# Kernel tuning notes

Measured on AMD Instinct MI355X. Metric: run time of the kernel, lower is better.

## Reference

```python
import jax, jax.numpy as jnp
import numpy as np

N_NODES = 50000
D_IN = 128
D_OUT = 64
N_ETYPES = 3
E_PER_ETYPE = 500000
P_ETYPE = 0.5  # self.p[etype] init value for every etype


def setup_inputs() -> dict:
    key = jax.random.key(0)
    k1, k2, k3, k4 = jax.random.split(key, 4)
    feat = jax.random.normal(k1, (N_NODES, D_IN), dtype=jnp.float32)
    W = jax.random.normal(k2, (D_IN, D_OUT), dtype=jnp.float32) * 0.05
    b = jax.random.normal(k3, (D_OUT,), dtype=jnp.float32) * 0.05
    # edge_index[e] = (src, dst) for etype e
    edge_index = jax.random.randint(k4, (N_ETYPES, 2, E_PER_ETYPE), 0, N_NODES, dtype=jnp.int64)
    return {"feat": feat, "W": W, "b": b, "edge_index": edge_index}


def reference(feat, W, b, edge_index):
    N = feat.shape[0]

    def agg_one_etype(ei):
        src, dst = ei[0], ei[1]
        # scatter-mean of src features onto dst nodes (dgl copy_u + mean)
        msg_sum = jax.ops.segment_sum(feat[src], dst, num_segments=N)          # [N, D]
        cnt = jax.ops.segment_sum(jnp.ones(src.shape, feat.dtype), dst, num_segments=N)
        hr = msg_sum / jnp.maximum(cnt, 1.0)[:, None]  # zero-in-degree nodes -> 0
        return jnp.tanh(hr)  # per-etype activation

    hr_all = jax.vmap(agg_one_etype)(edge_index)        # [n_etypes, N, D]
    h_homo = jnp.sum(hr_all * P_ETYPE, axis=0) + feat   # weighted sum + residual
    h_homo = jnp.tanh(h_homo)
    return h_homo @ W + b                               # final linear
```

## Files before the change

### kernel.cpp

```cpp
#include <hip/hip_runtime.h>
#include <hip/hip_bf16.h>

#define N_NODES 50000
#define D_IN 128
#define D_OUT 64
#define N_ETYPES 3
#define E_PER_ETYPE 500000
#define N_EDGES (N_ETYPES * E_PER_ETYPE)
#define CAP1 16
#define CAP2 30
#define DMAX (CAP1 + CAP2)
#define ZROW N_NODES
#define NB_FEAT ((N_NODES * D_IN / 4) / 256)
#define NB_W ((D_IN * D_OUT) / 256)
#define NB_ZCNT 147
#define CHUNK_EDGES 2048
#define N_CHUNKS ((N_EDGES + CHUNK_EDGES - 1) / CHUNK_EDGES)

typedef __attribute__((ext_vector_type(8))) short short8;
typedef __attribute__((ext_vector_type(4))) float f32x4;

static __device__ __forceinline__ unsigned short f2bf(float f) {
    unsigned int x = __float_as_uint(f);
    unsigned int lsb = (x >> 16) & 1u;
    x += 0x7fffu + lsb;
    return (unsigned short)(x >> 16);
}

static __device__ __forceinline__ float fast_tanh(float x) {
    float e = __expf(2.0f * x);
    return 1.0f - 2.0f * __builtin_amdgcn_rcpf(e + 1.0f);
}

static __device__ __forceinline__ short8 as_s8(uint4 u) {
    union { uint4 u; short8 s; } cv; cv.u = u; return cv.s;
}

static __device__ __forceinline__ void accum8(float* ax, uint4 p) {
    ax[0] += __uint_as_float(p.x << 16);
    ax[1] += __uint_as_float(p.x & 0xffff0000u);
    ax[2] += __uint_as_float(p.y << 16);
    ax[3] += __uint_as_float(p.y & 0xffff0000u);
    ax[4] += __uint_as_float(p.z << 16);
    ax[5] += __uint_as_float(p.z & 0xffff0000u);
    ax[6] += __uint_as_float(p.w << 16);
    ax[7] += __uint_as_float(p.w & 0xffff0000u);
}

static __device__ __forceinline__ float2 rs_reduce(const float* ax, int sub) {
    bool hi = (sub & 1);
    float k0_ = hi ? ax[4] : ax[0], s0_ = hi ? ax[0] : ax[4];
    float k1_ = hi ? ax[5] : ax[1], s1_ = hi ? ax[1] : ax[5];
    float k2_ = hi ? ax[6] : ax[2], s2_ = hi ? ax[2] : ax[6];
    float k3_ = hi ? ax[7] : ax[3], s3_ = hi ? ax[3] : ax[7];
    float h0 = k0_ + __shfl_xor(s0_, 16);
    float h1 = k1_ + __shfl_xor(s1_, 16);
    float h2 = k2_ + __shfl_xor(s2_, 16);
    float h3 = k3_ + __shfl_xor(s3_, 16);
    bool hi2 = (sub & 2);
    float ka = hi2 ? h2 : h0, sa = hi2 ? h0 : h2;
    float kb = hi2 ? h3 : h1, sb = hi2 ? h1 : h3;
    float2 v;
    v.x = ka + __shfl_xor(sa, 32);
    v.y = kb + __shfl_xor(sb, 32);
    return v;
}

__global__ __launch_bounds__(256) void convert_kernel(
    const float* __restrict__ feat,
    unsigned short* __restrict__ featbf,
    const float* __restrict__ W,
    unsigned short* __restrict__ wtbf,
    int* __restrict__ cnt)
{
    int b = blockIdx.x;
    if (b < NB_FEAT) {
        int i = b * 256 + threadIdx.x;
        const float4* f4 = (const float4*)feat;
        float4 v = f4[i];
        ushort4 o;
        o.x = f2bf(v.x); o.y = f2bf(v.y); o.z = f2bf(v.z); o.w = f2bf(v.w);
        ((ushort4*)featbf)[i] = o;
    } else if (b < NB_FEAT + NB_W) {
        int i = (b - NB_FEAT) * 256 + threadIdx.x;
        int n = i >> 7;
        int k = i & 127;
        wtbf[i] = f2bf(W[k * D_OUT + n]);
    } else if (b == NB_FEAT + NB_W) {
        if (threadIdx.x < 64)
            ((unsigned int*)(featbf + (size_t)N_NODES * D_IN))[threadIdx.x] = 0;
    } else {
        int i = (b - NB_FEAT - NB_W - 1) * 256 + threadIdx.x;
        if (i < (N_ETYPES * N_NODES) / 4) {
            int4 z; z.x = 0; z.y = 0; z.z = 0; z.w = 0;
            ((int4*)cnt)[i] = z;
        }
    }
}

__global__ __launch_bounds__(256) void fill_kernel(
    const int* __restrict__ edge_index,
    unsigned short* __restrict__ bucket1,
    unsigned short* __restrict__ spill,
    int* __restrict__ cnt)
{
    int slice = blockIdx.x & 7;
    int chunk = blockIdx.x >> 3;
    int e0 = chunk * CHUNK_EDGES + threadIdx.x;
    #pragma unroll
    for (int k = 0; k < CHUNK_EDGES / 256; k++) {
        int e = e0 + k * 256;
        if (e < N_EDGES) {
            int t  = e / E_PER_ETYPE;
            int ei = e - t * E_PER_ETYPE;
            const int* base = edge_index + (long long)t * 2 * E_PER_ETYPE;
            int dst = base[E_PER_ETYPE + ei];
            int s = (int)(((unsigned long long)(unsigned)dst * 687195ull) >> 32);
            if (s == slice) {
                int src = base[ei];
                int cell = t * N_NODES + dst;
                int pos = atomicAdd(cnt + cell, 1);
                if (pos < CAP1)
                    bucket1[cell * CAP1 + pos] = (unsigned short)src;
                else if (pos < CAP1 + CAP2)
                    spill[cell * CAP2 + (pos - CAP1)] = (unsigned short)src;
            }
        }
    }
}

__global__ __launch_bounds__(512) void gather_linear_kernel(
    const float* __restrict__ feat,
    const unsigned short* __restrict__ featbf,
    const unsigned short* __restrict__ wtbf,
    const float* __restrict__ bg,
    const unsigned short* __restrict__ bucket1,
    const unsigned short* __restrict__ spill,
    const int* __restrict__ cnt,
    float* __restrict__ out)
{
    __shared__ unsigned short hsb[16 * 128];

    int tid = threadIdx.x;
    int wave = tid >> 6;
    int lane = tid & 63;
    int sub  = lane >> 4;
    int sl   = lane & 15;
    int n0 = blockIdx.x * 16 + wave * 2;
    int n1 = n0 + 1;

    int degA[N_ETYPES], degB[N_ETYPES], idxA[N_ETYPES], idxB[N_ETYPES];
    #pragma unroll
    for (int t = 0; t < N_ETYPES; t++) {
        int cell = t * N_NODES + n0;
        int2 dg = *(const int2*)(cnt + cell);
        int la = 0, lb = 0;
        if (lane < CAP1) {
            la = bucket1[cell * CAP1 + lane];
            lb = bucket1[(cell + 1) * CAP1 + lane];
        } else if (lane < DMAX) {
            if (dg.x > CAP1) la = spill[cell * CAP2 + (lane - CAP1)];
            if (dg.y > CAP1) lb = spill[(cell + 1) * CAP2 + (lane - CAP1)];
        }
        int ca = dg.x < DMAX ? dg.x : DMAX;
        int cb = dg.y < DMAX ? dg.y : DMAX;
        idxA[t] = (lane < ca) ? la : ZROW;
        idxB[t] = (lane < cb) ? lb : ZROW;
        degA[t] = dg.x; degB[t] = dg.y;
    }

    int k0 = ((sub & 1) << 2) | (sub & 2);
    int p2 = 4 * sl + (k0 >> 1);
    float2 fA = ((const float2*)feat)[n0 * 64 + p2];
    float2 fB = ((const float2*)feat)[n1 * 64 + p2];

    const uint4* fb4 = (const uint4*)featbf;
    float s0A = 0.0f, s1A = 0.0f, s0B = 0.0f, s1B = 0.0f;

    #pragma unroll
    for (int t = 0; t < N_ETYPES; t++) {
        int da = degA[t] < DMAX ? degA[t] : DMAX;
        int db = degB[t] < DMAX ? degB[t] : DMAX;
        int dm = da > db ? da : db;
        float axA[8], axB[8];
        #pragma unroll
        for (int k = 0; k < 8; k++) { axA[k] = 0.0f; axB[k] = 0.0f; }
        for (int j = 0; j < dm; j += 8) {
            int r0 = j + sub;
            int r1 = j + 4 + sub;
            int sa0 = __shfl(idxA[t], r0);
            int sa1 = __shfl(idxA[t], r1);
            int sb0 = __shfl(idxB[t], r0);
            int sb1 = __shfl(idxB[t], r1);
            uint4 pa0 = fb4[sa0 * 16 + sl];
            uint4 pa1 = fb4[sa1 * 16 + sl];
            uint4 pb0 = fb4[sb0 * 16 + sl];
            uint4 pb1 = fb4[sb1 * 16 + sl];
            accum8(axA, pa0); accum8(axA, pa1);
            accum8(axB, pb0); accum8(axB, pb1);
        }
        float2 vA = rs_reduce(axA, sub);
        float2 vB = rs_reduce(axB, sub);
        float invA = __builtin_amdgcn_rcpf((float)(degA[t] > 0 ? degA[t] : 1));
        float invB = __builtin_amdgcn_rcpf((float)(degB[t] > 0 ? degB[t] : 1));
        s0A += fast_tanh(vA.x * invA);
        s1A += fast_tanh(vA.y * invA);
        s0B += fast_tanh(vB.x * invB);
        s1B += fast_tanh(vB.y * invB);
    }

    float hxA = fast_tanh(fA.x + 0.5f * s0A);
    float hyA = fast_tanh(fA.y + 0.5f * s1A);
    float hxB = fast_tanh(fB.x + 0.5f * s0B);
    float hyB = fast_tanh(fB.y + 0.5f * s1B);
    unsigned int hpA = (unsigned int)f2bf(hxA) | ((unsigned int)f2bf(hyA) << 16);
    unsigned int hpB = (unsigned int)f2bf(hxB) | ((unsigned int)f2bf(hyB) << 16);
    int colb = 16 * sl + 2 * k0;
    int rA = wave * 2, rB = rA + 1;
    ((unsigned int*)hsb)[(rA * 256 + (colb ^ ((rA & 7) << 4))) >> 2] = hpA;
    ((unsigned int*)hsb)[(rB * 256 + (colb ^ ((rB & 7) << 4))) >> 2] = hpB;

    uint4 b0 = {0,0,0,0}, b1 = {0,0,0,0}, b2 = {0,0,0,0}, b3 = {0,0,0,0};
    float bias = 0.0f;
    if (wave < 4) {
        int nrow = wave * 16 + sl;
        const uint4* wt4 = (const uint4*)wtbf;
        b0 = wt4[nrow * 16 +  0 + sub];
        b1 = wt4[nrow * 16 +  4 + sub];
        b2 = wt4[nrow * 16 +  8 + sub];
        b3 = wt4[nrow * 16 + 12 + sub];
        bias = bg[nrow];
    }
    __syncthreads();

    if (wave < 4) {
        int row = sl;
        int rbase = row * 256;
        int rx = (row & 7) << 4;
        const uint4* h4 = (const uint4*)hsb;
        uint4 a0 = h4[(rbase + (( 0 + sub * 16) ^ rx)) >> 4];
        uint4 a1 = h4[(rbase + (( 64 + sub * 16) ^ rx)) >> 4];
        uint4 a2 = h4[(rbase + ((128 + sub * 16) ^ rx)) >> 4];
        uint4 a3 = h4[(rbase + ((192 + sub * 16) ^ rx)) >> 4];

        f32x4 c = {bias, bias, bias, bias};
        c = __builtin_amdgcn_mfma_f32_16x16x32_bf16(as_s8(a0), as_s8(b0), c, 0, 0, 0);
        c = __builtin_amdgcn_mfma_f32_16x16x32_bf16(as_s8(a1), as_s8(b1), c, 0, 0, 0);
        c = __builtin_amdgcn_mfma_f32_16x16x32_bf16(as_s8(a2), as_s8(b2), c, 0, 0, 0);
        c = __builtin_amdgcn_mfma_f32_16x16x32_bf16(as_s8(a3), as_s8(b3), c, 0, 0, 0);

        #pragma unroll
        for (int i = 0; i < 4; i++) {
            int orow = sub * 4 + i;
            out[(blockIdx.x * 16 + orow) * 64 + wave * 16 + sl] = c[i];
        }
    }
}

extern "C" void kernel_launch(void* const* d_in, const int* in_sizes, int n_in,
                              void* d_out, int out_size, void* d_ws, size_t ws_size,
                              hipStream_t stream) {
    const float* feat = (const float*)d_in[0];
    const float* W    = (const float*)d_in[1];
    const float* b    = (const float*)d_in[2];
    const int* edge_index = (const int*)d_in[3];
    float* out = (float*)d_out;

    size_t featbf_bytes  = (size_t)(N_NODES + 1) * D_IN * sizeof(unsigned short);
    size_t bucket1_bytes = (size_t)N_ETYPES * N_NODES * CAP1 * sizeof(unsigned short);
    size_t spill_bytes   = (size_t)N_ETYPES * N_NODES * CAP2 * sizeof(unsigned short);
    size_t cnt_bytes     = (size_t)N_ETYPES * N_NODES * sizeof(int);
    size_t wtbf_bytes    = (size_t)D_IN * D_OUT * sizeof(unsigned short);
    if (ws_size < featbf_bytes + bucket1_bytes + spill_bytes + cnt_bytes + wtbf_bytes)
        return;

    unsigned short* featbf  = (unsigned short*)d_ws;
    unsigned short* bucket1 = (unsigned short*)((char*)d_ws + featbf_bytes);
    unsigned short* spill   = (unsigned short*)((char*)d_ws + featbf_bytes + bucket1_bytes);
    int* cnt = (int*)((char*)d_ws + featbf_bytes + bucket1_bytes + spill_bytes);
    unsigned short* wtbf = (unsigned short*)((char*)d_ws + featbf_bytes + bucket1_bytes
                                             + spill_bytes + cnt_bytes);

    convert_kernel<<<NB_FEAT + NB_W + 1 + NB_ZCNT, 256, 0, stream>>>(
        feat, featbf, W, wtbf, cnt);

    fill_kernel<<<N_CHUNKS * 8, 256, 0, stream>>>(edge_index, bucket1, spill, cnt);

    gather_linear_kernel<<<N_NODES / 16, 512, 0, stream>>>(
        feat, featbf, wtbf, b, bucket1, spill, cnt, out);
}
```

Before: 205.6 us.

## Replace sliced edge fill with two-phase partition-then-bin fill via per-slice queues

The single fill kernel, which had each of 8 slice blocks rescan every edge chunk, is replaced by two phases. A partition kernel reads each edge once, packs src, local dst and etype into a 32-bit record, and appends it to one of 8 per-slice queues using shared-memory counters plus one global atomic per slice per block. A binfill kernel then has blocks per slice walk their queue and do the bucket atomics, keeping atomics localized to each slice's dst range. This cuts the redundant edge-index reads at the cost of an extra queue write and read, an extra launch, and a fixed queue capacity (QCAP) that would silently drop edges if a slice overflows. It falls back to the old kernel when the workspace is too small.

```diff
diff --git a/kernel.cpp b/kernel.cpp
--- a/kernel.cpp
+++ b/kernel.cpp
@@ -13,9 +13,14 @@
 #define ZROW N_NODES
 #define NB_FEAT ((N_NODES * D_IN / 4) / 256)
 #define NB_W ((D_IN * D_OUT) / 256)
-#define NB_ZCNT 147
+#define NZINT4 ((N_ETYPES * N_NODES + 16) / 4)
+#define NB_ZCNT ((NZINT4 + 255) / 256)
 #define CHUNK_EDGES 2048
 #define N_CHUNKS ((N_EDGES + CHUNK_EDGES - 1) / CHUNK_EDGES)
+#define NSLICE 8
+#define SLICE_N 6250
+#define QCAP 196608
+#define NBLK_PER_SLICE 64
 
 typedef __attribute__((ext_vector_type(8))) short short8;
 typedef __attribute__((ext_vector_type(4))) float f32x4;
@@ -91,10 +96,80 @@
             ((unsigned int*)(featbf + (size_t)N_NODES * D_IN))[threadIdx.x] = 0;
     } else {
         int i = (b - NB_FEAT - NB_W - 1) * 256 + threadIdx.x;
-        if (i < (N_ETYPES * N_NODES) / 4) {
+        if (i < NZINT4) {
             int4 z; z.x = 0; z.y = 0; z.z = 0; z.w = 0;
             ((int4*)cnt)[i] = z;
         }
+    }
+}
+
+__global__ __launch_bounds__(256) void partition_kernel(
+    const int* __restrict__ edge_index,
+    unsigned int* __restrict__ queue,
+    int* __restrict__ qcnt)
+{
+    __shared__ int lcnt[NSLICE];
+    __shared__ int lbase[NSLICE];
+    int tid = threadIdx.x;
+    if (tid < NSLICE) lcnt[tid] = 0;
+    __syncthreads();
+
+    int e0 = blockIdx.x * CHUNK_EDGES + tid;
+    unsigned int rec[CHUNK_EDGES / 256];
+    int sl[CHUNK_EDGES / 256], pos[CHUNK_EDGES / 256];
+    #pragma unroll
+    for (int k = 0; k < CHUNK_EDGES / 256; k++) {
+        int e = e0 + k * 256;
+        sl[k] = -1;
+        if (e < N_EDGES) {
+            int t  = e / E_PER_ETYPE;
+            int ei = e - t * E_PER_ETYPE;
+            const int* base = edge_index + (long long)t * 2 * E_PER_ETYPE;
+            int src = __builtin_nontemporal_load(base + ei);
+            int dst = __builtin_nontemporal_load(base + E_PER_ETYPE + ei);
+            int s = (int)(((unsigned long long)(unsigned)dst * 687195ull) >> 32);
+            int ldst = dst - s * SLICE_N;
+            rec[k] = (unsigned)src | ((unsigned)ldst << 16) | ((unsigned)t << 29);
+            sl[k]  = s;
+            pos[k] = atomicAdd(&lcnt[s], 1);
+        }
+    }
+    __syncthreads();
+    if (tid < NSLICE) lbase[tid] = atomicAdd(&qcnt[tid], lcnt[tid]);
+    __syncthreads();
+    #pragma unroll
+    for (int k = 0; k < CHUNK_EDGES / 256; k++) {
+        if (sl[k] >= 0) {
+            int p = lbase[sl[k]] + pos[k];
+            if (p < QCAP)
+                queue[sl[k] * QCAP + p] = rec[k];
+        }
+    }
+}
+
+__global__ __launch_bounds__(256) void binfill_kernel(
+    const unsigned int* __restrict__ queue,
+    const int* __restrict__ qcnt,
+    unsigned short* __restrict__ bucket1,
+    unsigned short* __restrict__ spill,
+    int* __restrict__ cnt)
+{
+    int slice = blockIdx.x & 7;
+    int blk   = blockIdx.x >> 3;
+    int total = qcnt[slice];
+    const unsigned int* q = queue + slice * QCAP;
+    int sbase = slice * SLICE_N;
+    for (int i = blk * 256 + threadIdx.x; i < total; i += NBLK_PER_SLICE * 256) {
+        unsigned int r = __builtin_nontemporal_load(q + i);
+        int src  = r & 0xFFFF;
+        int ldst = (r >> 16) & 0x1FFF;
+        int t    = r >> 29;
+        int cell = t * N_NODES + sbase + ldst;
+        int p = atomicAdd(cnt + cell, 1);
+        if (p < CAP1)
+            bucket1[cell * CAP1 + p] = (unsigned short)src;
+        else if (p < DMAX)
+            spill[cell * CAP2 + (p - CAP1)] = (unsigned short)src;
     }
 }
 
@@ -269,22 +344,33 @@
     size_t featbf_bytes  = (size_t)(N_NODES + 1) * D_IN * sizeof(unsigned short);
     size_t bucket1_bytes = (size_t)N_ETYPES * N_NODES * CAP1 * sizeof(unsigned short);
     size_t spill_bytes   = (size_t)N_ETYPES * N_NODES * CAP2 * sizeof(unsigned short);
-    size_t cnt_bytes     = (size_t)N_ETYPES * N_NODES * sizeof(int);
+    size_t cnt_bytes     = (size_t)(N_ETYPES * N_NODES + 16) * sizeof(int);
     size_t wtbf_bytes    = (size_t)D_IN * D_OUT * sizeof(unsigned short);
-    if (ws_size < featbf_bytes + bucket1_bytes + spill_bytes + cnt_bytes + wtbf_bytes)
+    size_t base_bytes    = featbf_bytes + bucket1_bytes + spill_bytes + cnt_bytes + wtbf_bytes;
+    size_t queue_bytes   = (size_t)NSLICE * QCAP * sizeof(unsigned int);
+    if (ws_size < base_bytes)
         return;
+    bool twophase = (ws_size >= base_bytes + queue_bytes);
 
     unsigned short* featbf  = (unsigned short*)d_ws;
     unsigned short* bucket1 = (unsigned short*)((char*)d_ws + featbf_bytes);
     unsigned short* spill   = (unsigned short*)((char*)d_ws + featbf_bytes + bucket1_bytes);
     int* cnt = (int*)((char*)d_ws + featbf_bytes + bucket1_bytes + spill_bytes);
+    int* qcnt = cnt + N_ETYPES * N_NODES;
     unsigned short* wtbf = (unsigned short*)((char*)d_ws + featbf_bytes + bucket1_bytes
                                              + spill_bytes + cnt_bytes);
+    unsigned int* queue = (unsigned int*)((char*)d_ws + base_bytes);
 
     convert_kernel<<<NB_FEAT + NB_W + 1 + NB_ZCNT, 256, 0, stream>>>(
         feat, featbf, W, wtbf, cnt);
 
-    fill_kernel<<<N_CHUNKS * 8, 256, 0, stream>>>(edge_index, bucket1, spill, cnt);
+    if (twophase) {
+        partition_kernel<<<N_CHUNKS, 256, 0, stream>>>(edge_index, queue, qcnt);
+        binfill_kernel<<<NSLICE * NBLK_PER_SLICE, 256, 0, stream>>>(
+            queue, qcnt, bucket1, spill, cnt);
+    } else {
+        fill_kernel<<<N_CHUNKS * 8, 256, 0, stream>>>(edge_index, bucket1, spill, cnt);
+    }
 
     gather_linear_kernel<<<N_NODES / 16, 512, 0, stream>>>(
         feat, featbf, wtbf, b, bucket1, spill, cnt, out);
```

Result: slower. 216.0 us (+5.0%).
